# Optimization experiments

Measured on AMD Instinct MI355X. Metric: run time of the kernel, lower is better.

The kernel has to match this reference:

```python
import math
import jax, jax.numpy as jnp
import numpy as np

# ---------- real Wigner 3j (e3nn convention, unit Frobenius norm) ----------
def _su2_cg(j1, j2, j3):
    def f(n):
        return math.factorial(round(n))
    mat = np.zeros((2 * j1 + 1, 2 * j2 + 1, 2 * j3 + 1))
    for m1 in range(-j1, j1 + 1):
        for m2 in range(-j2, j2 + 1):
            m3 = m1 + m2
            if abs(m3) > j3:
                continue
            vmin = max(-j1 + j2 + m3, -j1 + m1, 0)
            vmax = min(j2 + j3 + m1, j3 - j1 + j2, j3 + m3)
            C = math.sqrt((2 * j3 + 1) * f(j3 + j1 - j2) * f(j3 - j1 + j2) * f(j1 + j2 - j3)
                          * f(j3 + m3) * f(j3 - m3)
                          / (f(j1 + j2 + j3 + 1) * f(j1 - m1) * f(j1 + m1) * f(j2 - m2) * f(j2 + m2)))
            S = 0.0
            for v in range(vmin, vmax + 1):
                S += (-1) ** (v + j2 + m2) * f(j2 + j3 + m1 - v) * f(j1 - m1 + v) / (
                    f(v) * f(j3 - j1 + j2 - v) * f(j3 + m3 - v) * f(v + j1 - j2 - m3))
            mat[j1 + m1, j2 + m2, j3 + m3] = C * S
    return mat

def _real_to_complex(l):
    q = np.zeros((2 * l + 1, 2 * l + 1), dtype=np.complex128)
    for m in range(-l, 0):
        q[l + m, l + abs(m)] = 1.0 / math.sqrt(2)
        q[l + m, l - abs(m)] = -1j / math.sqrt(2)
    q[l, l] = 1.0
    for m in range(1, l + 1):
        q[l + m, l + abs(m)] = (-1) ** m / math.sqrt(2)
        q[l + m, l - abs(m)] = 1j * (-1) ** m / math.sqrt(2)
    return (-1j) ** l * q

def _wigner_3j(l1, l2, l3):
    Q1, Q2, Q3 = _real_to_complex(l1), _real_to_complex(l2), _real_to_complex(l3)
    C = _su2_cg(l1, l2, l3).astype(np.complex128)
    C = np.einsum('ij,kl,mn,ikn->jlm', Q1, Q2, np.conj(Q3.T), C).real
    return (C / np.linalg.norm(C)).astype(np.float32)

# ---------- architecture constants (from init_kwargs) ----------
IRREPS_NODE = [(128, 0), (64, 1), (32, 2)]   # 128x0e+64x1e+32x2e, dim 480
IRREPS_EDGE = [(1, 0), (1, 1), (1, 2)]       # 1x0e+1x1e+1x2e (spherical harmonics), dim 9
OUT_LS = (0, 1, 2)
N_NODES, N_EDGES, N_BASIS = 10000, 80000, 128
FC_HIDDEN = 64
AVG_AGG = 8.0
NODE_DIM = sum(m * (2 * l + 1) for m, l in IRREPS_NODE)  # 480

# uvu instructions: (i, l1, j, l2, l3, mul); kept if ir_out in output irreps or 0e
INSTRUCTIONS = []
for _i, (_mul, _l1) in enumerate(IRREPS_NODE):
    for _j, (_, _l2) in enumerate(IRREPS_EDGE):
        for _l3 in range(abs(_l1 - _l2), _l1 + _l2 + 1):
            if _l3 in OUT_LS:
                INSTRUCTIONS.append((_i, _l1, _j, _l2, _l3, _mul))
WEIGHT_NUMEL = sum(ins[5] for ins in INSTRUCTIONS)                       # 960
CAT_MULS = {l: sum(ins[5] for ins in INSTRUCTIONS if ins[4] == l) for l in OUT_LS}  # {0:224,1:384,2:352}
W3J = {(l1, l2, l3): jnp.asarray(_wigner_3j(l1, l2, l3))
       for (_, l1, _, l2, l3, _) in INSTRUCTIONS}

def _layernorm(x, g, b):
    mu = jnp.mean(x, axis=-1, keepdims=True)
    var = jnp.mean((x - mu) ** 2, axis=-1, keepdims=True)
    return (x - mu) * jax.lax.rsqrt(var + 1e-5) * g + b

def _forward(node_input, edge_attr, edge_scalars, edge_src, edge_dst,
             exp_w, exp_b, rad_w1, rad_b1, rad_ln1_g, rad_ln1_b,
             rad_w2, rad_b2, rad_ln2_g, rad_ln2_b, rad_w3, rad_offset,
             proj_w0, proj_w1, proj_w2, proj_b):
    N = node_input.shape[0]
    E = edge_attr.shape[0]
    dt = node_input.dtype
    # exp: LinearRS('1x0e' -> irreps) applied to all-ones scalars; only 0e channels populated
    node0 = jnp.broadcast_to(exp_w + exp_b, (N, IRREPS_NODE[0][0]))   # [N,128]
    xs = [node0[edge_src][:, :, None],                                # [E,128,1] gather by edge_src
          jnp.zeros((E, IRREPS_NODE[1][0], 3), dt),                   # 1e block (structurally zero)
          jnp.zeros((E, IRREPS_NODE[2][0], 5), dt)]                   # 2e block (structurally zero)
    ys = [edge_attr[:, 0:1], edge_attr[:, 1:4], edge_attr[:, 4:9]]
    # radial MLP -> per-edge TP weights [E, 960]
    h = jax.nn.silu(_layernorm(edge_scalars @ rad_w1 + rad_b1, rad_ln1_g, rad_ln1_b))
    h = jax.nn.silu(_layernorm(h @ rad_w2 + rad_b2, rad_ln2_g, rad_ln2_b))
    w = h @ rad_w3 + rad_offset
    # depthwise ('uvu') CG tensor product, outputs grouped by l (even-first sort; all even here)
    per_l = {l: [] for l in OUT_LS}
    off = 0
    for (i, l1, j, l2, l3, mul) in INSTRUCTIONS:
        w_ins = w[:, off:off + mul]   # [E, mul] (v = 1)
        off += mul
        cg = W3J[(l1, l2, l3)] * math.sqrt(2 * l3 + 1)
        per_l[l3].append(jnp.einsum('ijk,eui,ej,eu->euk', cg, xs[i], ys[j], w_ins))
    cat = {l: jnp.concatenate(per_l[l], axis=1) for l in OUT_LS}      # [E, CAT_MULS[l], 2l+1]
    # proj: e3nn Linear (per-l multiplicity mixing; bias on scalars only)
    p0 = jnp.einsum('eui,uo->eoi', cat[0], proj_w0) + proj_b[None, :, None]
    p1 = jnp.einsum('eui,uo->eoi', cat[1], proj_w1)
    p2 = jnp.einsum('eui,uo->eoi', cat[2], proj_w2)
    edge_feat = jnp.concatenate([p0.reshape(E, -1), p1.reshape(E, -1), p2.reshape(E, -1)], axis=1)  # [E,480]
    # scaled scatter-add over destination nodes
    out = jax.ops.segment_sum(edge_feat, edge_dst, num_segments=N)
    return out / math.sqrt(AVG_AGG)

def setup_inputs() -> dict:
    key = jax.random.key(0)
    ks = jax.random.split(key, 16)
    f32 = jnp.float32
    inv = lambda n: 1.0 / math.sqrt(n)
    return {
        'node_input': jax.random.normal(ks[0], (N_NODES, NODE_DIM), f32),
        'edge_attr': jax.random.normal(ks[1], (N_EDGES, 9), f32),
        'edge_scalars': jax.random.uniform(ks[2], (N_EDGES, N_BASIS), f32),
        'edge_src': jax.random.randint(ks[3], (N_EDGES,), 0, N_NODES),
        'edge_dst': jax.random.randint(ks[4], (N_EDGES,), 0, N_NODES),
        'batch': jnp.zeros((N_NODES,), jnp.int32),
        'exp_w': jax.random.normal(ks[5], (128,), f32),
        'exp_b': jnp.zeros((128,), f32),
        'rad_w1': jax.random.normal(ks[6], (N_BASIS, FC_HIDDEN), f32) * inv(N_BASIS),
        'rad_b1': jnp.zeros((FC_HIDDEN,), f32),
        'rad_ln1_g': jnp.ones((FC_HIDDEN,), f32),
        'rad_ln1_b': jnp.zeros((FC_HIDDEN,), f32),
        'rad_w2': jax.random.normal(ks[7], (FC_HIDDEN, FC_HIDDEN), f32) * inv(FC_HIDDEN),
        'rad_b2': jnp.zeros((FC_HIDDEN,), f32),
        'rad_ln2_g': jnp.ones((FC_HIDDEN,), f32),
        'rad_ln2_b': jnp.zeros((FC_HIDDEN,), f32),
        'rad_w3': jax.random.normal(ks[8], (FC_HIDDEN, WEIGHT_NUMEL), f32) * inv(FC_HIDDEN),
        'rad_offset': jax.random.normal(ks[9], (WEIGHT_NUMEL,), f32) * 0.1,
        'proj_w0': jax.random.normal(ks[10], (CAT_MULS[0], 128), f32) * inv(CAT_MULS[0]),
        'proj_w1': jax.random.normal(ks[11], (CAT_MULS[1], 64), f32) * inv(CAT_MULS[1]),
        'proj_w2': jax.random.normal(ks[12], (CAT_MULS[2], 32), f32) * inv(CAT_MULS[2]),
        'proj_b': jnp.zeros((128,), f32),
    }

def reference(node_input, edge_attr, edge_scalars, edge_src, edge_dst, batch,
              exp_w, exp_b, rad_w1, rad_b1, rad_ln1_g, rad_ln1_b,
              rad_w2, rad_b2, rad_ln2_g, rad_ln2_b, rad_w3, rad_offset,
              proj_w0, proj_w1, proj_w2, proj_b):
    return _forward(node_input, edge_attr, edge_scalars, edge_src, edge_dst,
                    exp_w, exp_b, rad_w1, rad_b1, rad_ln1_g, rad_ln1_b,
                    rad_w2, rad_b2, rad_ln2_g, rad_ln2_b, rad_w3, rad_offset,
                    proj_w0, proj_w1, proj_w2, proj_b)
```

## Files before the change

kernel.cpp:

```cpp
#include <hip/hip_runtime.h>
#include <math.h>


#define NEDGES 80000
#define NNODES 10000
#define NPAD   10048
#define NB_L0  157
#define NB_L12 313

__device__ __forceinline__ float silu_f(float y) {
    return y / (1.0f + __expf(-y));
}

__global__ __launch_bounds__(256) void precompute_and_hist(
    const float* __restrict__ exp_w, const float* __restrict__ exp_b,
    const float* __restrict__ rad_w3,
    const float* __restrict__ rad_offset,
    const float* __restrict__ proj_w0,
    const float* __restrict__ proj_w1,
    const float* __restrict__ proj_w2,
    float* __restrict__ M, float* __restrict__ cvec,
    const int* __restrict__ edge_dst, int* __restrict__ counts)
{
    if (blockIdx.x >= 65) {
        int b = blockIdx.x - 65;
        for (int e = b * 256 + threadIdx.x; e < NEDGES; e += 100 * 256)
            atomicAdd(&counts[edge_dst[e]], 1);
        return;
    }
    __shared__ float x0[128];
    int t = threadIdx.x;
    if (t < 128) x0[t] = exp_w[t] + exp_b[t];
    __syncthreads();
    if (t >= 224) return;
    int h = blockIdx.x;
    const float* src = (h < 64) ? (rad_w3 + h * 960) : rad_offset;
    float acc = 0.0f;
    if (t < 128) {
#pragma unroll 4
        for (int u = 0; u < 128; ++u) acc += src[u] * x0[u] * proj_w0[u * 128 + t];
    } else if (t < 192) {
        int o = t - 128;
#pragma unroll 4
        for (int u = 0; u < 128; ++u) acc += src[128 + u] * x0[u] * proj_w1[u * 64 + o];
    } else {
        int o = t - 192;
#pragma unroll 4
        for (int u = 0; u < 128; ++u) acc += src[256 + u] * x0[u] * proj_w2[u * 32 + o];
    }
    if (h < 64) M[h * 224 + t] = acc;
    else        cvec[t] = acc;
}

__global__ __launch_bounds__(1024) void scan_counts(
    int* __restrict__ counts, int* __restrict__ offsets)
{
    __shared__ int wsum[16];
    const int t = threadIdx.x;
    const int lane = t & 63, w = t >> 6;
    const int base = t * 10;
    int local[10];
    int s = 0;
#pragma unroll
    for (int i = 0; i < 10; ++i) {
        int idx = base + i;
        int v = (idx < NNODES) ? counts[idx] : 0;
        local[i] = s;
        s += v;
    }
    int incl = s;
#pragma unroll
    for (int off = 1; off < 64; off <<= 1) {
        int up = __shfl_up(incl, off, 64);
        if (lane >= off) incl += up;
    }
    if (lane == 63) wsum[w] = incl;
    __syncthreads();
    if (t < 16) {
        int v = wsum[t];
#pragma unroll
        for (int off = 1; off < 16; off <<= 1) {
            int up = __shfl_up(v, off, 64);
            if (t >= off) v += up;
        }
        wsum[t] = v;
    }
    __syncthreads();
    int wbase = (w == 0) ? 0 : wsum[w - 1];
    int excl = wbase + incl - s;
#pragma unroll
    for (int i = 0; i < 10; ++i) {
        int idx = base + i;
        if (idx < NNODES) {
            offsets[idx] = excl + local[i];
            counts[idx] = 0;
        }
    }
    if (t == 1023) offsets[NNODES] = excl + s;
}

__global__ __launch_bounds__(256) void edge_h2(
    const float* __restrict__ edge_scalars,
    const int*   __restrict__ edge_dst,
    const int*   __restrict__ offsets,
    int*         __restrict__ cursor,
    const float* __restrict__ rad_w1,
    const float* __restrict__ rad_b1,
    const float* __restrict__ g1, const float* __restrict__ bt1,
    const float* __restrict__ rad_w2,
    const float* __restrict__ rad_b2,
    const float* __restrict__ g2, const float* __restrict__ bt2,
    float* __restrict__ h2csr,
    int*   __restrict__ order)
{
    __shared__ float S[16384 + 64];
    float* W1s = S;
    float* W2s = S + 8192;
    float* ES  = S + 12288;
    int*   pos_s = (int*)(S + 16384);

    const int t    = threadIdx.x;
    const int lane = t & 63;
    const int wid  = t >> 6;
    const int er   = lane & 3;
    const int cc   = lane >> 2;
    const int eb   = blockIdx.x * 64;

    {
        const float4* s1 = (const float4*)rad_w1;
        float4* d1 = (float4*)W1s;
#pragma unroll
        for (int i = 0; i < 8; ++i) d1[t + i * 256] = s1[t + i * 256];
        const float4* s2 = (const float4*)rad_w2;
        float4* d2 = (float4*)W2s;
#pragma unroll
        for (int i = 0; i < 4; ++i) d2[t + i * 256] = s2[t + i * 256];
    }
    if (t < 64) {
        int e = eb + t;
        int d = edge_dst[e];
        int p = offsets[d] + atomicAdd(&cursor[d], 1);
        order[p] = e;
        pos_s[t] = p;
    }
    {
        const int re = t >> 2, seg = t & 3;
        const float* row = edge_scalars + (size_t)(eb + re) * 128;
#pragma unroll
        for (int q = 0; q < 4; ++q) {
            float4 v = *(const float4*)(row + seg * 16 + q * 4);
            ES[(seg * 16 + q * 4 + 0) * 64 + re] = v.x;
            ES[(seg * 16 + q * 4 + 1) * 64 + re] = v.y;
            ES[(seg * 16 + q * 4 + 2) * 64 + re] = v.z;
            ES[(seg * 16 + q * 4 + 3) * 64 + re] = v.w;
        }
    }
    __syncthreads();

    const int n0 = cc * 4;
    float b1v[4], g1v[4], t1v[4], b2v[4], g2v[4], t2v[4];
#pragma unroll
    for (int j = 0; j < 4; ++j) {
        b1v[j] = rad_b1[n0 + j]; g1v[j] = g1[n0 + j]; t1v[j] = bt1[n0 + j];
        b2v[j] = rad_b2[n0 + j]; g2v[j] = g2[n0 + j]; t2v[j] = bt2[n0 + j];
    }

    float acc[4][4];
#pragma unroll
    for (int i = 0; i < 4; ++i)
#pragma unroll
        for (int j = 0; j < 4; ++j) acc[i][j] = b1v[j];

    const int ecol = wid * 16 + er * 4;

#pragma unroll 8
    for (int k = 0; k < 64; ++k) {
        float4 av = *(const float4*)&ES[k * 64 + ecol];
        float4 wv = *(const float4*)&W1s[k * 64 + n0];
        float a4[4] = {av.x, av.y, av.z, av.w};
        float w4[4] = {wv.x, wv.y, wv.z, wv.w};
#pragma unroll
        for (int i = 0; i < 4; ++i)
#pragma unroll
            for (int j = 0; j < 4; ++j) acc[i][j] = fmaf(a4[i], w4[j], acc[i][j]);
    }
    __syncthreads();
    {
        const int re = t >> 2, seg = t & 3;
        const float* row = edge_scalars + (size_t)(eb + re) * 128 + 64;
#pragma unroll
        for (int q = 0; q < 4; ++q) {
            float4 v = *(const float4*)(row + seg * 16 + q * 4);
            ES[(seg * 16 + q * 4 + 0) * 64 + re] = v.x;
            ES[(seg * 16 + q * 4 + 1) * 64 + re] = v.y;
            ES[(seg * 16 + q * 4 + 2) * 64 + re] = v.z;
            ES[(seg * 16 + q * 4 + 3) * 64 + re] = v.w;
        }
    }
    __syncthreads();
#pragma unroll 8
    for (int k = 0; k < 64; ++k) {
        float4 av = *(const float4*)&ES[k * 64 + ecol];
        float4 wv = *(const float4*)&W1s[(64 + k) * 64 + n0];
        float a4[4] = {av.x, av.y, av.z, av.w};
        float w4[4] = {wv.x, wv.y, wv.z, wv.w};
#pragma unroll
        for (int i = 0; i < 4; ++i)
#pragma unroll
            for (int j = 0; j < 4; ++j) acc[i][j] = fmaf(a4[i], w4[j], acc[i][j]);
    }
    __syncthreads();

    float* H = W1s + wid * 1280;
    {
        float s1i[4], s2i[4];
#pragma unroll
        for (int i = 0; i < 4; ++i) {
            s1i[i] = acc[i][0] + acc[i][1] + acc[i][2] + acc[i][3];
            s2i[i] = acc[i][0] * acc[i][0] + acc[i][1] * acc[i][1]
                   + acc[i][2] * acc[i][2] + acc[i][3] * acc[i][3];
        }
#pragma unroll
        for (int m = 4; m <= 32; m <<= 1) {
#pragma unroll
            for (int i = 0; i < 4; ++i) {
                s1i[i] += __shfl_xor(s1i[i], m, 64);
                s2i[i] += __shfl_xor(s2i[i], m, 64);
            }
        }
#pragma unroll
        for (int i = 0; i < 4; ++i) {
            float mu  = s1i[i] * (1.0f / 64.0f);
            float var = s2i[i] * (1.0f / 64.0f) - mu * mu;
            float rs  = rsqrtf(var + 1e-5f);
#pragma unroll
            for (int j = 0; j < 4; ++j) {
                float y = (acc[i][j] - mu) * rs * g1v[j] + t1v[j];
                H[(n0 + j) * 20 + er * 4 + i] = silu_f(y);
            }
        }
    }

    float acc2[4][4];
#pragma unroll
    for (int i = 0; i < 4; ++i)
#pragma unroll
        for (int j = 0; j < 4; ++j) acc2[i][j] = b2v[j];
#pragma unroll 8
    for (int u = 0; u < 64; ++u) {
        float4 hv = *(const float4*)&H[u * 20 + er * 4];
        float4 wv = *(const float4*)&W2s[u * 64 + n0];
        float h4[4] = {hv.x, hv.y, hv.z, hv.w};
        float w4[4] = {wv.x, wv.y, wv.z, wv.w};
#pragma unroll
        for (int i = 0; i < 4; ++i)
#pragma unroll
            for (int j = 0; j < 4; ++j) acc2[i][j] = fmaf(h4[i], w4[j], acc2[i][j]);
    }

    {
        float s1i[4], s2i[4];
#pragma unroll
        for (int i = 0; i < 4; ++i) {
            s1i[i] = acc2[i][0] + acc2[i][1] + acc2[i][2] + acc2[i][3];
            s2i[i] = acc2[i][0] * acc2[i][0] + acc2[i][1] * acc2[i][1]
                   + acc2[i][2] * acc2[i][2] + acc2[i][3] * acc2[i][3];
        }
#pragma unroll
        for (int m = 4; m <= 32; m <<= 1) {
#pragma unroll
            for (int i = 0; i < 4; ++i) {
                s1i[i] += __shfl_xor(s1i[i], m, 64);
                s2i[i] += __shfl_xor(s2i[i], m, 64);
            }
        }
#pragma unroll
        for (int i = 0; i < 4; ++i) {
            float mu  = s1i[i] * (1.0f / 64.0f);
            float var = s2i[i] * (1.0f / 64.0f) - mu * mu;
            float rs  = rsqrtf(var + 1e-5f);
            float4 v;
            v.x = silu_f((acc2[i][0] - mu) * rs * g2v[0] + t2v[0]);
            v.y = silu_f((acc2[i][1] - mu) * rs * g2v[1] + t2v[1]);
            v.z = silu_f((acc2[i][2] - mu) * rs * g2v[2] + t2v[2]);
            v.w = silu_f((acc2[i][3] - mu) * rs * g2v[3] + t2v[3]);
            *(float4*)&ES[(wid * 16 + er * 4 + i) * 64 + n0] = v;
        }
    }
    __syncthreads();

    {
        const int r = t >> 2, p = t & 3;
        int pos = pos_s[r];
        float* dst = h2csr + (size_t)pos * 64 + p * 16;
        const float* src = &ES[r * 64 + p * 16];
#pragma unroll
        for (int q = 0; q < 4; ++q)
            *(float4*)(dst + q * 4) = *(const float4*)(src + q * 4);
    }
}

__global__ __launch_bounds__(1024) void t_build(
    const float* __restrict__ h2csr,
    const float* __restrict__ edge_attr,
    const int*   __restrict__ order,
    const int*   __restrict__ offsets,
    float* __restrict__ Tbuf,
    float* __restrict__ ysb)
{
    const int lane = threadIdx.x & 63;
    const int n = __builtin_amdgcn_readfirstlane(blockIdx.x * 16 + (threadIdx.x >> 6));
    const int s0 = offsets[n], s1 = offsets[n + 1];

    float T[9]  = {0, 0, 0, 0, 0, 0, 0, 0, 0};
    float ys[9] = {0, 0, 0, 0, 0, 0, 0, 0, 0};
    for (int i = s0; i < s1; ++i) {
        float hv = h2csr[(size_t)i * 64 + lane];
        int e = order[i];
        const float* ya = edge_attr + (size_t)e * 9;
#pragma unroll
        for (int k = 0; k < 9; ++k) {
            float y = ya[k];
            T[k] += hv * y;
            ys[k] += y;
        }
    }
    float* tb = Tbuf + (size_t)n * 576;
#pragma unroll
    for (int k = 0; k < 9; ++k) tb[k * 64 + lane] = T[k];
#pragma unroll
    for (int k = 0; k < 9; ++k) if (lane == k) ysb[n * 9 + k] = ys[k];
}

__global__ __launch_bounds__(256) void proj(
    const float* __restrict__ Tbuf, const float* __restrict__ ysb,
    const int*   __restrict__ offsets,
    const float* __restrict__ M,
    const float* __restrict__ cvec,
    const float* __restrict__ proj_b,
    float* __restrict__ out)
{
    __shared__ float S[13248];
    const int tid = threadIdx.x;
    const int bid = blockIdx.x;
    constexpr float inv = 0.35355339059327373f;

    if (bid < NB_L0) {
        const int n0 = bid * 64;
        for (int it = tid; it < 1024; it += 256) {
            int ni = it >> 4, q4 = it & 15;
            float4 v = *(const float4*)&Tbuf[(size_t)(n0 + ni) * 576 + q4 * 4];
            S[(q4 * 4 + 0) * 66 + ni] = v.x;
            S[(q4 * 4 + 1) * 66 + ni] = v.y;
            S[(q4 * 4 + 2) * 66 + ni] = v.z;
            S[(q4 * 4 + 3) * 66 + ni] = v.w;
        }
        for (int it = tid; it < 2048; it += 256) {
            int u = it >> 5, c4 = it & 31;
            *(float4*)&S[4224 + u * 128 + c4 * 4] = *(const float4*)&M[u * 224 + c4 * 4];
        }
        __syncthreads();
        const int np = tid & 15, cg = tid >> 4;
        float acc[4][8];
#pragma unroll
        for (int i = 0; i < 4; ++i)
#pragma unroll
            for (int j = 0; j < 8; ++j) acc[i][j] = 0.0f;
#pragma unroll 4
        for (int u = 0; u < 64; ++u) {
            float4 tv = *(const float4*)&S[u * 66 + np * 4];
            float4 m0 = *(const float4*)&S[4224 + u * 128 + cg * 8];
            float4 m1 = *(const float4*)&S[4224 + u * 128 + cg * 8 + 4];
            float ta[4] = {tv.x, tv.y, tv.z, tv.w};
            float ma[8] = {m0.x, m0.y, m0.z, m0.w, m1.x, m1.y, m1.z, m1.w};
#pragma unroll
            for (int i = 0; i < 4; ++i)
#pragma unroll
                for (int j = 0; j < 8; ++j) acc[i][j] = fmaf(ta[i], ma[j], acc[i][j]);
        }
#pragma unroll
        for (int i = 0; i < 4; ++i) {
            int n = n0 + np * 4 + i;
            if (n >= NNODES) continue;
            float ys0 = ysb[n * 9];
            float cnt = (float)(offsets[n + 1] - offsets[n]);
            float f[8];
#pragma unroll
            for (int j = 0; j < 8; ++j) {
                int col = cg * 8 + j;
                f[j] = (acc[i][j] + cvec[col] * ys0 + cnt * proj_b[col]) * inv;
            }
            *(float4*)&out[(size_t)n * 480 + cg * 8]     = *(float4*)&f[0];
            *(float4*)&out[(size_t)n * 480 + cg * 8 + 4] = *(float4*)&f[4];
        }
    } else if (bid < NB_L0 + NB_L12) {
        const int n0 = (bid - NB_L0) * 32;
        for (int it = tid; it < 1536; it += 256) {
            int r = it >> 4, q4 = it & 15;
            int kq = r >> 5, ni = r & 31;
            float4 v = *(const float4*)&Tbuf[(size_t)(n0 + ni) * 576 + (1 + kq) * 64 + q4 * 4];
            float* dst = &S[kq * 2176];
            dst[(q4 * 4 + 0) * 34 + ni] = v.x;
            dst[(q4 * 4 + 1) * 34 + ni] = v.y;
            dst[(q4 * 4 + 2) * 34 + ni] = v.z;
            dst[(q4 * 4 + 3) * 34 + ni] = v.w;
        }
        for (int it = tid; it < 1024; it += 256) {
            int u = it >> 4, c4 = it & 15;
            *(float4*)&S[6528 + u * 64 + c4 * 4] = *(const float4*)&M[u * 224 + 128 + c4 * 4];
        }
        __syncthreads();
        const int np = tid & 15, cg = tid >> 4;
        float acc[2][4][3];
#pragma unroll
        for (int i = 0; i < 2; ++i)
#pragma unroll
            for (int j = 0; j < 4; ++j)
#pragma unroll
                for (int kq = 0; kq < 3; ++kq) acc[i][j][kq] = 0.0f;
#pragma unroll 4
        for (int u = 0; u < 64; ++u) {
            float2 t0 = *(const float2*)&S[0 * 2176 + u * 34 + np * 2];
            float2 t1 = *(const float2*)&S[1 * 2176 + u * 34 + np * 2];
            float2 t2 = *(const float2*)&S[2 * 2176 + u * 34 + np * 2];
            float4 m  = *(const float4*)&S[6528 + u * 64 + cg * 4];
            float ma[4] = {m.x, m.y, m.z, m.w};
            float ta[2][3] = {{t0.x, t1.x, t2.x}, {t0.y, t1.y, t2.y}};
#pragma unroll
            for (int i = 0; i < 2; ++i)
#pragma unroll
                for (int j = 0; j < 4; ++j) {
                    acc[i][j][0] = fmaf(ta[i][0], ma[j], acc[i][j][0]);
                    acc[i][j][1] = fmaf(ta[i][1], ma[j], acc[i][j][1]);
                    acc[i][j][2] = fmaf(ta[i][2], ma[j], acc[i][j][2]);
                }
        }
#pragma unroll
        for (int i = 0; i < 2; ++i) {
            int n = n0 + np * 2 + i;
            if (n >= NNODES) continue;
            float y1 = ysb[n * 9 + 1], y2 = ysb[n * 9 + 2], y3 = ysb[n * 9 + 3];
            float f[12];
#pragma unroll
            for (int j = 0; j < 4; ++j) {
                int cc = cg * 4 + j;
                float cv = cvec[128 + cc];
                f[j * 3 + 0] = (acc[i][j][0] + cv * y1) * inv;
                f[j * 3 + 1] = (acc[i][j][1] + cv * y2) * inv;
                f[j * 3 + 2] = (acc[i][j][2] + cv * y3) * inv;
            }
            float* dst = &out[(size_t)n * 480 + 128 + cg * 12];
            *(float4*)(dst + 0) = *(float4*)&f[0];
            *(float4*)(dst + 4) = *(float4*)&f[4];
            *(float4*)(dst + 8) = *(float4*)&f[8];
        }
    } else {
        const int n0 = (bid - NB_L0 - NB_L12) * 32;
        for (int it = tid; it < 2560; it += 256) {
            int r = it >> 4, q4 = it & 15;
            int kq = r >> 5, ni = r & 31;
            float4 v = *(const float4*)&Tbuf[(size_t)(n0 + ni) * 576 + (4 + kq) * 64 + q4 * 4];
            float* dst = &S[kq * 2176];
            dst[(q4 * 4 + 0) * 34 + ni] = v.x;
            dst[(q4 * 4 + 1) * 34 + ni] = v.y;
            dst[(q4 * 4 + 2) * 34 + ni] = v.z;
            dst[(q4 * 4 + 3) * 34 + ni] = v.w;
        }
        for (int it = tid; it < 512; it += 256) {
            int u = it >> 3, c4 = it & 7;
            *(float4*)&S[10880 + u * 32 + c4 * 4] = *(const float4*)&M[u * 224 + 192 + c4 * 4];
        }
        __syncthreads();
        const int np = tid & 15, cg = tid >> 4;
        float acc[2][2][5];
#pragma unroll
        for (int i = 0; i < 2; ++i)
#pragma unroll
            for (int j = 0; j < 2; ++j)
#pragma unroll
                for (int kq = 0; kq < 5; ++kq) acc[i][j][kq] = 0.0f;
#pragma unroll 4
        for (int u = 0; u < 64; ++u) {
            float2 tq[5];
#pragma unroll
            for (int kq = 0; kq < 5; ++kq)
                tq[kq] = *(const float2*)&S[kq * 2176 + u * 34 + np * 2];
            float2 m = *(const float2*)&S[10880 + u * 32 + cg * 2];
            float ma[2] = {m.x, m.y};
#pragma unroll
            for (int i = 0; i < 2; ++i) {
                float ti[5] = {(&tq[0].x)[i], (&tq[1].x)[i], (&tq[2].x)[i],
                               (&tq[3].x)[i], (&tq[4].x)[i]};
#pragma unroll
                for (int j = 0; j < 2; ++j)
#pragma unroll
                    for (int kq = 0; kq < 5; ++kq)
                        acc[i][j][kq] = fmaf(ti[kq], ma[j], acc[i][j][kq]);
            }
        }
#pragma unroll
        for (int i = 0; i < 2; ++i) {
            int n = n0 + np * 2 + i;
            if (n >= NNODES) continue;
            float yk[5];
#pragma unroll
            for (int kq = 0; kq < 5; ++kq) yk[kq] = ysb[n * 9 + 4 + kq];
            float f[10];
#pragma unroll
            for (int j = 0; j < 2; ++j) {
                int cc = cg * 2 + j;
                float cv = cvec[192 + cc];
#pragma unroll
                for (int kq = 0; kq < 5; ++kq)
                    f[j * 5 + kq] = (acc[i][j][kq] + cv * yk[kq]) * inv;
            }
            float* dst = &out[(size_t)n * 480 + 320 + cg * 10];
#pragma unroll
            for (int q = 0; q < 5; ++q)
                *(float2*)(dst + q * 2) = *(float2*)&f[q * 2];
        }
    }
}

extern "C" void kernel_launch(void* const* d_in, const int* in_sizes, int n_in,
                              void* d_out, int out_size, void* d_ws, size_t ws_size,
                              hipStream_t stream)
{
    const float* edge_attr    = (const float*)d_in[1];
    const float* edge_scalars = (const float*)d_in[2];
    const int*   edge_dst     = (const int*)d_in[4];
    const float* exp_w   = (const float*)d_in[6];
    const float* exp_b   = (const float*)d_in[7];
    const float* rad_w1  = (const float*)d_in[8];
    const float* rad_b1  = (const float*)d_in[9];
    const float* g1      = (const float*)d_in[10];
    const float* bt1     = (const float*)d_in[11];
    const float* rad_w2  = (const float*)d_in[12];
    const float* rad_b2  = (const float*)d_in[13];
    const float* g2      = (const float*)d_in[14];
    const float* bt2     = (const float*)d_in[15];
    const float* rad_w3  = (const float*)d_in[16];
    const float* rad_off = (const float*)d_in[17];
    const float* pw0     = (const float*)d_in[18];
    const float* pw1     = (const float*)d_in[19];
    const float* pw2     = (const float*)d_in[20];
    const float* proj_b  = (const float*)d_in[21];

    float* M       = (float*)d_ws;
    float* cvec    = M + 14336;
    float* h2csr   = cvec + 224;
    int*   counts  = (int*)(h2csr + (size_t)NEDGES * 64);
    int*   offsets = counts + NNODES;
    int*   order   = offsets + NNODES + 1;
    float* Tbuf    = (float*)(order + NEDGES);
    float* ysb     = Tbuf + (size_t)NPAD * 576;

    hipMemsetAsync(counts, 0, NNODES * sizeof(int), stream);
    precompute_and_hist<<<165, 256, 0, stream>>>(exp_w, exp_b, rad_w3, rad_off,
        pw0, pw1, pw2, M, cvec, edge_dst, counts);
    scan_counts<<<1, 1024, 0, stream>>>(counts, offsets);
    edge_h2<<<NEDGES / 64, 256, 0, stream>>>(edge_scalars, edge_dst,
        offsets, counts, rad_w1, rad_b1, g1, bt1, rad_w2, rad_b2, g2, bt2,
        h2csr, order);
    t_build<<<NNODES / 16, 1024, 0, stream>>>(h2csr, edge_attr, order,
        offsets, Tbuf, ysb);
    proj<<<NB_L0 + 2 * NB_L12, 256, 0, stream>>>(Tbuf, ysb, offsets,
        M, cvec, proj_b, (float*)d_out);
}
```

Before: 112.1 us.

## Retile radial MLP to 8x8 per-thread register blocks with per-wave edge tiles

The edge MLP kernel now uses 128-thread blocks where each wave owns 64 edges and each thread computes an 8x8 output tile instead of 4x4. This raises FMA-to-LDS-load ratio and removes most block-level barriers in favour of per-wave waitcnt fences. The hidden layer is stored in an XOR-swizzled layout to avoid bank conflicts, and outputs go straight to the CSR buffer via a shuffled position. Costs include higher register pressure (two 64-float accumulators) and larger shared memory per block, which may lower occupancy; relying on wave-local lgkmcnt waits instead of barriers is also fragile.

```diff
diff --git a/kernel.cpp b/kernel.cpp
--- a/kernel.cpp
+++ b/kernel.cpp
@@ -99,7 +99,7 @@
     if (t == 1023) offsets[NNODES] = excl + s;
 }
 
-__global__ __launch_bounds__(256) void edge_h2(
+__global__ __launch_bounds__(128) void edge_h2(
     const float* __restrict__ edge_scalars,
     const int*   __restrict__ edge_dst,
     const int*   __restrict__ offsets,
@@ -113,190 +113,182 @@
     float* __restrict__ h2csr,
     int*   __restrict__ order)
 {
-    __shared__ float S[16384 + 64];
-    float* W1s = S;
-    float* W2s = S + 8192;
-    float* ES  = S + 12288;
-    int*   pos_s = (int*)(S + 16384);
+    __shared__ float W1s[128 * 64];
+    __shared__ float W2s[64 * 64];
+    __shared__ float ES[2][64 * 64];
 
     const int t    = threadIdx.x;
     const int lane = t & 63;
     const int wid  = t >> 6;
-    const int er   = lane & 3;
-    const int cc   = lane >> 2;
-    const int eb   = blockIdx.x * 64;
+    const int er   = lane & 7;
+    const int cc   = lane >> 3;
+    const int n0   = cc * 8;
+    const int we0  = (blockIdx.x * 2 + wid) * 64;
+    float* ESw = ES[wid];
 
     {
         const float4* s1 = (const float4*)rad_w1;
         float4* d1 = (float4*)W1s;
 #pragma unroll
-        for (int i = 0; i < 8; ++i) d1[t + i * 256] = s1[t + i * 256];
+        for (int i = 0; i < 16; ++i) d1[t + i * 128] = s1[t + i * 128];
         const float4* s2 = (const float4*)rad_w2;
         float4* d2 = (float4*)W2s;
 #pragma unroll
-        for (int i = 0; i < 4; ++i) d2[t + i * 256] = s2[t + i * 256];
-    }
-    if (t < 64) {
-        int e = eb + t;
-        int d = edge_dst[e];
-        int p = offsets[d] + atomicAdd(&cursor[d], 1);
-        order[p] = e;
-        pos_s[t] = p;
-    }
+        for (int i = 0; i < 8; ++i) d2[t + i * 128] = s2[t + i * 128];
+    }
+
+    const int e_own = we0 + lane;
+    int posv;
     {
-        const int re = t >> 2, seg = t & 3;
-        const float* row = edge_scalars + (size_t)(eb + re) * 128;
-#pragma unroll
-        for (int q = 0; q < 4; ++q) {
-            float4 v = *(const float4*)(row + seg * 16 + q * 4);
-            ES[(seg * 16 + q * 4 + 0) * 64 + re] = v.x;
-            ES[(seg * 16 + q * 4 + 1) * 64 + re] = v.y;
-            ES[(seg * 16 + q * 4 + 2) * 64 + re] = v.z;
-            ES[(seg * 16 + q * 4 + 3) * 64 + re] = v.w;
-        }
+        int d = edge_dst[e_own];
+        posv = offsets[d] + atomicAdd(&cursor[d], 1);
+        order[posv] = e_own;
     }
     __syncthreads();
 
-    const int n0 = cc * 4;
-    float b1v[4], g1v[4], t1v[4], b2v[4], g2v[4], t2v[4];
-#pragma unroll
-    for (int j = 0; j < 4; ++j) {
+    float b1v[8], g1v[8], t1v[8], b2v[8], g2v[8], t2v[8];
+#pragma unroll
+    for (int j = 0; j < 8; ++j) {
         b1v[j] = rad_b1[n0 + j]; g1v[j] = g1[n0 + j]; t1v[j] = bt1[n0 + j];
         b2v[j] = rad_b2[n0 + j]; g2v[j] = g2[n0 + j]; t2v[j] = bt2[n0 + j];
     }
 
-    float acc[4][4];
-#pragma unroll
-    for (int i = 0; i < 4; ++i)
-#pragma unroll
-        for (int j = 0; j < 4; ++j) acc[i][j] = b1v[j];
-
-    const int ecol = wid * 16 + er * 4;
-
-#pragma unroll 8
-    for (int k = 0; k < 64; ++k) {
-        float4 av = *(const float4*)&ES[k * 64 + ecol];
-        float4 wv = *(const float4*)&W1s[k * 64 + n0];
-        float a4[4] = {av.x, av.y, av.z, av.w};
-        float w4[4] = {wv.x, wv.y, wv.z, wv.w};
-#pragma unroll
-        for (int i = 0; i < 4; ++i)
-#pragma unroll
-            for (int j = 0; j < 4; ++j) acc[i][j] = fmaf(a4[i], w4[j], acc[i][j]);
-    }
-    __syncthreads();
+    float acc[8][8];
+#pragma unroll
+    for (int i = 0; i < 8; ++i)
+#pragma unroll
+        for (int j = 0; j < 8; ++j) acc[i][j] = b1v[j];
+
+    const int rl = lane >> 1, cl = lane & 1;
+#pragma unroll
+    for (int h = 0; h < 2; ++h) {
+#pragma unroll
+        for (int p = 0; p < 2; ++p) {
+            const float* row = edge_scalars
+                + (size_t)(we0 + p * 32 + rl) * 128 + h * 64 + cl * 4;
+            const int e = p * 32 + rl;
+#pragma unroll
+            for (int q = 0; q < 8; ++q) {
+                float4 v = *(const float4*)(row + q * 8);
+                const int kb = cl * 4 + q * 8;
+                ESw[(kb + 0) * 64 + e] = v.x;
+                ESw[(kb + 1) * 64 + e] = v.y;
+                ESw[(kb + 2) * 64 + e] = v.z;
+                ESw[(kb + 3) * 64 + e] = v.w;
+            }
+        }
+        asm volatile("s_waitcnt lgkmcnt(0)" ::: "memory");
+
+#pragma unroll 4
+        for (int k = 0; k < 64; ++k) {
+            float4 avA = *(const float4*)&ESw[k * 64 + er * 8];
+            float4 avB = *(const float4*)&ESw[k * 64 + er * 8 + 4];
+            float4 wvA = *(const float4*)&W1s[(h * 64 + k) * 64 + n0];
+            float4 wvB = *(const float4*)&W1s[(h * 64 + k) * 64 + n0 + 4];
+            float a8[8] = {avA.x, avA.y, avA.z, avA.w, avB.x, avB.y, avB.z, avB.w};
+            float w8[8] = {wvA.x, wvA.y, wvA.z, wvA.w, wvB.x, wvB.y, wvB.z, wvB.w};
+#pragma unroll
+            for (int i = 0; i < 8; ++i)
+#pragma unroll
+                for (int j = 0; j < 8; ++j)
+                    acc[i][j] = fmaf(a8[i], w8[j], acc[i][j]);
+        }
+        asm volatile("s_waitcnt lgkmcnt(0)" ::: "memory");
+    }
+
     {
-        const int re = t >> 2, seg = t & 3;
-        const float* row = edge_scalars + (size_t)(eb + re) * 128 + 64;
-#pragma unroll
-        for (int q = 0; q < 4; ++q) {
-            float4 v = *(const float4*)(row + seg * 16 + q * 4);
-            ES[(seg * 16 + q * 4 + 0) * 64 + re] = v.x;
-            ES[(seg * 16 + q * 4 + 1) * 64 + re] = v.y;
-            ES[(seg * 16 + q * 4 + 2) * 64 + re] = v.z;
-            ES[(seg * 16 + q * 4 + 3) * 64 + re] = v.w;
-        }
-    }
-    __syncthreads();
-#pragma unroll 8
-    for (int k = 0; k < 64; ++k) {
-        float4 av = *(const float4*)&ES[k * 64 + ecol];
-        float4 wv = *(const float4*)&W1s[(64 + k) * 64 + n0];
-        float a4[4] = {av.x, av.y, av.z, av.w};
-        float w4[4] = {wv.x, wv.y, wv.z, wv.w};
-#pragma unroll
-        for (int i = 0; i < 4; ++i)
-#pragma unroll
-            for (int j = 0; j < 4; ++j) acc[i][j] = fmaf(a4[i], w4[j], acc[i][j]);
-    }
-    __syncthreads();
-
-    float* H = W1s + wid * 1280;
+        float s1[8], s2[8];
+#pragma unroll
+        for (int i = 0; i < 8; ++i) {
+            float a = 0.0f, b = 0.0f;
+#pragma unroll
+            for (int j = 0; j < 8; ++j) { a += acc[i][j]; b = fmaf(acc[i][j], acc[i][j], b); }
+            s1[i] = a; s2[i] = b;
+        }
+#pragma unroll
+        for (int m = 8; m <= 32; m <<= 1) {
+#pragma unroll
+            for (int i = 0; i < 8; ++i) {
+                s1[i] += __shfl_xor(s1[i], m, 64);
+                s2[i] += __shfl_xor(s2[i], m, 64);
+            }
+        }
+        const int sw = ((cc >> 1) & 3) << 1;
+#pragma unroll
+        for (int i = 0; i < 8; ++i) {
+            float mu  = s1[i] * (1.0f / 64.0f);
+            float var = s2[i] * (1.0f / 64.0f) - mu * mu;
+            float rs  = rsqrtf(var + 1e-5f);
+#pragma unroll
+            for (int j = 0; j < 8; ++j) {
+                float y = (acc[i][j] - mu) * rs * g1v[j] + t1v[j];
+                ESw[(n0 + j) * 64 + ((er * 8 + i) ^ sw)] = silu_f(y);
+            }
+        }
+    }
+    asm volatile("s_waitcnt lgkmcnt(0)" ::: "memory");
+
+    float acc2[8][8];
+#pragma unroll
+    for (int i = 0; i < 8; ++i)
+#pragma unroll
+        for (int j = 0; j < 8; ++j) acc2[i][j] = b2v[j];
+
+#pragma unroll
+    for (int ur = 0; ur < 4; ++ur) {
+        const int usw = ur << 1;
+#pragma unroll 4
+        for (int uu = 0; uu < 16; ++uu) {
+            const int u = ur * 16 + uu;
+            float4 avA = *(const float4*)&ESw[u * 64 + er * 8];
+            float4 avB = *(const float4*)&ESw[u * 64 + er * 8 + 4];
+            float tmp[8] = {avA.x, avA.y, avA.z, avA.w, avB.x, avB.y, avB.z, avB.w};
+            float4 wvA = *(const float4*)&W2s[u * 64 + n0];
+            float4 wvB = *(const float4*)&W2s[u * 64 + n0 + 4];
+            float w8[8] = {wvA.x, wvA.y, wvA.z, wvA.w, wvB.x, wvB.y, wvB.z, wvB.w};
+#pragma unroll
+            for (int i = 0; i < 8; ++i) {
+                float hv = tmp[i ^ usw];
+#pragma unroll
+                for (int j = 0; j < 8; ++j)
+                    acc2[i][j] = fmaf(hv, w8[j], acc2[i][j]);
+            }
+        }
+    }
+
     {
-        float s1i[4], s2i[4];
-#pragma unroll
-        for (int i = 0; i < 4; ++i) {
-            s1i[i] = acc[i][0] + acc[i][1] + acc[i][2] + acc[i][3];
-            s2i[i] = acc[i][0] * acc[i][0] + acc[i][1] * acc[i][1]
-                   + acc[i][2] * acc[i][2] + acc[i][3] * acc[i][3];
-        }
-#pragma unroll
-        for (int m = 4; m <= 32; m <<= 1) {
-#pragma unroll
-            for (int i = 0; i < 4; ++i) {
-                s1i[i] += __shfl_xor(s1i[i], m, 64);
-                s2i[i] += __shfl_xor(s2i[i], m, 64);
-            }
-        }
-#pragma unroll
-        for (int i = 0; i < 4; ++i) {
-            float mu  = s1i[i] * (1.0f / 64.0f);
-            float var = s2i[i] * (1.0f / 64.0f) - mu * mu;
+        float s1[8], s2[8];
+#pragma unroll
+        for (int i = 0; i < 8; ++i) {
+            float a = 0.0f, b = 0.0f;
+#pragma unroll
+            for (int j = 0; j < 8; ++j) { a += acc2[i][j]; b = fmaf(acc2[i][j], acc2[i][j], b); }
+            s1[i] = a; s2[i] = b;
+        }
+#pragma unroll
+        for (int m = 8; m <= 32; m <<= 1) {
+#pragma unroll
+            for (int i = 0; i < 8; ++i) {
+                s1[i] += __shfl_xor(s1[i], m, 64);
+                s2[i] += __shfl_xor(s2[i], m, 64);
+            }
+        }
+#pragma unroll
+        for (int i = 0; i < 8; ++i) {
+            float mu  = s1[i] * (1.0f / 64.0f);
+            float var = s2[i] * (1.0f / 64.0f) - mu * mu;
             float rs  = rsqrtf(var + 1e-5f);
-#pragma unroll
-            for (int j = 0; j < 4; ++j) {
-                float y = (acc[i][j] - mu) * rs * g1v[j] + t1v[j];
-                H[(n0 + j) * 20 + er * 4 + i] = silu_f(y);
-            }
-        }
-    }
-
-    float acc2[4][4];
-#pragma unroll
-    for (int i = 0; i < 4; ++i)
-#pragma unroll
-        for (int j = 0; j < 4; ++j) acc2[i][j] = b2v[j];
-#pragma unroll 8
-    for (int u = 0; u < 64; ++u) {
-        float4 hv = *(const float4*)&H[u * 20 + er * 4];
-        float4 wv = *(const float4*)&W2s[u * 64 + n0];
-        float h4[4] = {hv.x, hv.y, hv.z, hv.w};
-        float w4[4] = {wv.x, wv.y, wv.z, wv.w};
-#pragma unroll
-        for (int i = 0; i < 4; ++i)
-#pragma unroll
-            for (int j = 0; j < 4; ++j) acc2[i][j] = fmaf(h4[i], w4[j], acc2[i][j]);
-    }
-
-    {
-        float s1i[4], s2i[4];
-#pragma unroll
-        for (int i = 0; i < 4; ++i) {
-            s1i[i] = acc2[i][0] + acc2[i][1] + acc2[i][2] + acc2[i][3];
-            s2i[i] = acc2[i][0] * acc2[i][0] + acc2[i][1] * acc2[i][1]
-                   + acc2[i][2] * acc2[i][2] + acc2[i][3] * acc2[i][3];
-        }
-#pragma unroll
-        for (int m = 4; m <= 32; m <<= 1) {
-#pragma unroll
-            for (int i = 0; i < 4; ++i) {
-                s1i[i] += __shfl_xor(s1i[i], m, 64);
-                s2i[i] += __shfl_xor(s2i[i], m, 64);
-            }
-        }
-#pragma unroll
-        for (int i = 0; i < 4; ++i) {
-            float mu  = s1i[i] * (1.0f / 64.0f);
-            float var = s2i[i] * (1.0f / 64.0f) - mu * mu;
-            float rs  = rsqrtf(var + 1e-5f);
-            float4 v;
-            v.x = silu_f((acc2[i][0] - mu) * rs * g2v[0] + t2v[0]);
-            v.y = silu_f((acc2[i][1] - mu) * rs * g2v[1] + t2v[1]);
-            v.z = silu_f((acc2[i][2] - mu) * rs * g2v[2] + t2v[2]);
-            v.w = silu_f((acc2[i][3] - mu) * rs * g2v[3] + t2v[3]);
-            *(float4*)&ES[(wid * 16 + er * 4 + i) * 64 + n0] = v;
-        }
-    }
-    __syncthreads();
-
-    {
-        const int r = t >> 2, p = t & 3;
-        int pos = pos_s[r];
-        float* dst = h2csr + (size_t)pos * 64 + p * 16;
-        const float* src = &ES[r * 64 + p * 16];
-#pragma unroll
-        for (int q = 0; q < 4; ++q)
-            *(float4*)(dst + q * 4) = *(const float4*)(src + q * 4);
+            float f[8];
+#pragma unroll
+            for (int j = 0; j < 8; ++j) {
+                float y = (acc2[i][j] - mu) * rs * g2v[j] + t2v[j];
+                f[j] = silu_f(y);
+            }
+            int pe = __shfl(posv, er * 8 + i, 64);
+            float* dst = h2csr + (size_t)pe * 64 + n0;
+            *(float4*)(dst)     = *(float4*)&f[0];
+            *(float4*)(dst + 4) = *(float4*)&f[4];
+        }
     }
 }
 
@@ -559,7 +551,7 @@
     precompute_and_hist<<<165, 256, 0, stream>>>(exp_w, exp_b, rad_w3, rad_off,
         pw0, pw1, pw2, M, cvec, edge_dst, counts);
     scan_counts<<<1, 1024, 0, stream>>>(counts, offsets);
-    edge_h2<<<NEDGES / 64, 256, 0, stream>>>(edge_scalars, edge_dst,
+    edge_h2<<<NEDGES / 128, 128, 0, stream>>>(edge_scalars, edge_dst,
         offsets, counts, rad_w1, rad_b1, g1, bt1, rad_w2, rad_b2, g2, bt2,
         h2csr, order);
     t_build<<<NNODES / 16, 1024, 0, stream>>>(h2csr, edge_attr, order,
```

Result: slower. 129.8 us (+15.8%).
